# Kernel tuning notes

Measured on AMD Instinct MI355X. Metric: run time of the kernel, lower is better.

## Reference

```python
import jax, jax.numpy as jnp
import numpy as np
import math

B, S, D = 32, 512, 1024
H = 16
DH = D // H
L = 4
DFF = 2048
DMEM = 512
EPS = 1e-5


def _pos_encoding(seq_len, d_model):
    # sinusoidal PE, shape [seq_len, 1, d_model]
    position = jnp.arange(seq_len, dtype=jnp.float32)[:, None]
    div_term = jnp.exp(jnp.arange(0, d_model, 2, dtype=jnp.float32) * (-math.log(10000.0) / d_model))
    pe = jnp.zeros((seq_len, d_model), dtype=jnp.float32)
    pe = pe.at[:, 0::2].set(jnp.sin(position * div_term))
    pe = pe.at[:, 1::2].set(jnp.cos(position * div_term))
    return pe[:, None, :]


def _layer_norm(x, g, b):
    mu = jnp.mean(x, axis=-1, keepdims=True)
    var = jnp.mean(jnp.square(x - mu), axis=-1, keepdims=True)
    return (x - mu) * jax.lax.rsqrt(var + EPS) * g + b


def setup_inputs() -> dict:
    key = jax.random.key(0)
    ks = jax.random.split(key, 8)
    w = 0.02  # weight scale for stable deep stack
    return {
        "x": jax.random.normal(ks[0], (B, S, D), dtype=jnp.float32),
        "Wqkv": jax.random.normal(ks[1], (L, 3 * D, D), dtype=jnp.float32) * w,
        "bqkv": jnp.zeros((L, 3 * D), dtype=jnp.float32),
        "Wo": jax.random.normal(ks[2], (L, D, D), dtype=jnp.float32) * w,
        "bo": jnp.zeros((L, D), dtype=jnp.float32),
        "W1": jax.random.normal(ks[3], (L, DFF, D), dtype=jnp.float32) * w,
        "b1": jnp.zeros((L, DFF), dtype=jnp.float32),
        "W2": jax.random.normal(ks[4], (L, D, DFF), dtype=jnp.float32) * w,
        "b2": jnp.zeros((L, D), dtype=jnp.float32),
        "ln1_g": jnp.ones((L, D), dtype=jnp.float32),
        "ln1_b": jnp.zeros((L, D), dtype=jnp.float32),
        "ln2_g": jnp.ones((L, D), dtype=jnp.float32),
        "ln2_b": jnp.zeros((L, D), dtype=jnp.float32),
        "normf_g": jnp.ones((D,), dtype=jnp.float32),
        "normf_b": jnp.zeros((D,), dtype=jnp.float32),
        "Wout": jax.random.normal(ks[5], (DMEM, D), dtype=jnp.float32) * w,
        "bout": jnp.zeros((DMEM,), dtype=jnp.float32),
    }


def reference(x, Wqkv, bqkv, Wo, bo, W1, b1, W2, b2,
              ln1_g, ln1_b, ln2_g, ln2_b, normf_g, normf_b, Wout, bout):
    # x: [B, S, D] -> [S, B, D]
    h = jnp.transpose(x, (1, 0, 2))
    h = h + _pos_encoding(S, D)  # dropout p=0 in eval
    scale = 1.0 / math.sqrt(DH)
    for l in range(L):
        # --- self-attention block (post-norm) ---
        qkv = h @ Wqkv[l].T + bqkv[l]          # [S, B, 3D]
        q, k, v = jnp.split(qkv, 3, axis=-1)
        q = q.reshape(S, B, H, DH)
        k = k.reshape(S, B, H, DH)
        v = v.reshape(S, B, H, DH)
        scores = jnp.einsum('sbhd,tbhd->bhst', q, k) * scale  # [B, H, S, S]
        attn = jax.nn.softmax(scores, axis=-1)
        ctx = jnp.einsum('bhst,tbhd->sbhd', attn, v).reshape(S, B, D)
        sa = ctx @ Wo[l].T + bo[l]
        h = _layer_norm(h + sa, ln1_g[l], ln1_b[l])
        # --- feed-forward block (post-norm) ---
        ff = jax.nn.relu(h @ W1[l].T + b1[l]) @ W2[l].T + b2[l]
        h = _layer_norm(h + ff, ln2_g[l], ln2_b[l])
    h = _layer_norm(h, normf_g, normf_b)       # encoder final norm
    h = jnp.transpose(h, (1, 0, 2))            # [B, S, D]
    return h @ Wout.T + bout                   # [B, S, DMEM]
```

## Files before the change

kernel.cpp:

```cpp
#include <hip/hip_runtime.h>

#define BB    32
#define SS    512
#define DD    1024
#define HH_   16
#define DH    64
#define LL    4
#define DFF   2048
#define DMEM  512
#define NTOK  (BB * SS)
#define SPLD  74

typedef __attribute__((ext_vector_type(8))) short short8;
typedef __attribute__((ext_vector_type(4))) float f32x4;

__device__ __forceinline__ unsigned short f2bf(float x) {
    unsigned u = __float_as_uint(x);
    u = (u + 0x7FFFu + ((u >> 16) & 1u)) >> 16;
    return (unsigned short)u;
}
__device__ __forceinline__ float bf2f(unsigned short x) {
    return __uint_as_float(((unsigned)x) << 16);
}

__device__ __forceinline__ void async16(const unsigned short* g, unsigned short* l) {
    __builtin_amdgcn_global_load_lds(
        (__attribute__((address_space(1))) void*)g,
        (__attribute__((address_space(3))) void*)l,
        16, 0, 0);
}

__global__ void cvt_bf16(const float* __restrict__ in, unsigned short* __restrict__ out, int n) {
    int i4 = (blockIdx.x * 256 + threadIdx.x) * 4;
    if (i4 < n) {
        float4 v = *(const float4*)&in[i4];
        uint2 pk;
        pk.x = f2bf(v.x) | ((unsigned)f2bf(v.y) << 16);
        pk.y = f2bf(v.z) | ((unsigned)f2bf(v.w) << 16);
        *(uint2*)&out[i4] = pk;
    }
}

__global__ void add_pe_kernel(const float* __restrict__ x,
                              unsigned short* __restrict__ hb) {
    int i4 = (blockIdx.x * 256 + threadIdx.x) * 4;
    int d = i4 & (DD - 1);
    int t = i4 >> 10;
    int s = t & (SS - 1);
    const float c = -9.210340371976184f / (float)DD;
    float f0 = __expf((float)d * c);
    float f2 = __expf((float)(d + 2) * c);
    float a0 = (float)s * f0, a2 = (float)s * f2;
    float4 xv = *(const float4*)&x[i4];
    uint2 pk;
    pk.x = f2bf(xv.x + __sinf(a0)) | ((unsigned)f2bf(xv.y + __cosf(a0)) << 16);
    pk.y = f2bf(xv.z + __sinf(a2)) | ((unsigned)f2bf(xv.w + __cosf(a2)) << 16);
    *(uint2*)&hb[i4] = pk;
}

#define BAR   __builtin_amdgcn_s_barrier()
#define LGKM0 do { asm volatile("s_waitcnt lgkmcnt(0)" ::: "memory"); \
                   __builtin_amdgcn_sched_barrier(0); } while (0)
#define VMC8  asm volatile("s_waitcnt vmcnt(8)" ::: "memory")

#define STAGE(BUF, OP, HALFI, KS) do {                                          \
    const unsigned short* _g = (OP) ? Wb : A;                                   \
    const size_t _gr = ((OP) ? Brow0 : Arow0) + (HALFI) * 128 + wid * 16 + l8;  \
    unsigned short* _d = &lds[BUF][OP][(((HALFI) * 128 + wid * 16)) * 64];      \
    const int _ks = (KS);                                                       \
    async16(&_g[_gr * (size_t)K + _ks + cl8], _d);                              \
    async16(&_g[(_gr + 8) * (size_t)K + _ks + cl8], _d + 8 * 64);               \
} while (0)

#define HALF_ITER(CUR, KSR) {                                                   \
    short8 afr[4][2], b01[2][2], b23[2][2];                                     \
    _Pragma("unroll") for (int m = 0; m < 4; m++) {                             \
        afr[m][0] = *(const short8*)&lds[CUR][0][aro + m * 1024 + cb0];         \
        afr[m][1] = *(const short8*)&lds[CUR][0][aro + m * 1024 + cb1]; }       \
    _Pragma("unroll") for (int n = 0; n < 2; n++) {                             \
        b01[n][0] = *(const short8*)&lds[CUR][1][bro + n * 1024 + cb0];         \
        b01[n][1] = *(const short8*)&lds[CUR][1][bro + n * 1024 + cb1]; }       \
    BAR; LGKM0;                                                                 \
    __builtin_amdgcn_s_setprio(1);                                              \
    _Pragma("unroll") for (int m = 0; m < 4; m++)                               \
        _Pragma("unroll") for (int n = 0; n < 2; n++) {                         \
            acc[m][n] = __builtin_amdgcn_mfma_f32_16x16x32_bf16(b01[n][0], afr[m][0], acc[m][n], 0, 0, 0); \
            acc[m][n] = __builtin_amdgcn_mfma_f32_16x16x32_bf16(b01[n][1], afr[m][1], acc[m][n], 0, 0, 0); } \
    __builtin_amdgcn_s_setprio(0);                                              \
    BAR;                                                                        \
    _Pragma("unroll") for (int n = 0; n < 2; n++) {                             \
        b23[n][0] = *(const short8*)&lds[CUR][1][bro + (n + 2) * 1024 + cb0];   \
        b23[n][1] = *(const short8*)&lds[CUR][1][bro + (n + 2) * 1024 + cb1]; } \
    BAR; LGKM0;                                                                 \
    __builtin_amdgcn_s_setprio(1);                                              \
    _Pragma("unroll") for (int m = 0; m < 4; m++)                               \
        _Pragma("unroll") for (int n = 0; n < 2; n++) {                         \
            acc[m][n + 2] = __builtin_amdgcn_mfma_f32_16x16x32_bf16(b23[n][0], afr[m][0], acc[m][n + 2], 0, 0, 0); \
            acc[m][n + 2] = __builtin_amdgcn_mfma_f32_16x16x32_bf16(b23[n][1], afr[m][1], acc[m][n + 2], 0, 0, 0); } \
    __builtin_amdgcn_s_setprio(0);                                              \
    BAR;                                                                        \
    _Pragma("unroll") for (int m = 0; m < 4; m++) {                             \
        afr[m][0] = *(const short8*)&lds[CUR][0][aro + (m + 4) * 1024 + cb0];   \
        afr[m][1] = *(const short8*)&lds[CUR][0][aro + (m + 4) * 1024 + cb1]; } \
    STAGE(CUR, 1, 0, KSR);                                                      \
    STAGE(CUR, 1, 1, KSR);                                                      \
    BAR; LGKM0;                                                                 \
    __builtin_amdgcn_s_setprio(1);                                              \
    _Pragma("unroll") for (int m = 0; m < 4; m++)                               \
        _Pragma("unroll") for (int n = 0; n < 2; n++) {                         \
            acc[m + 4][n + 2] = __builtin_amdgcn_mfma_f32_16x16x32_bf16(b23[n][0], afr[m][0], acc[m + 4][n + 2], 0, 0, 0); \
            acc[m + 4][n + 2] = __builtin_amdgcn_mfma_f32_16x16x32_bf16(b23[n][1], afr[m][1], acc[m + 4][n + 2], 0, 0, 0); } \
    __builtin_amdgcn_s_setprio(0);                                              \
    BAR;                                                                        \
    STAGE(CUR, 0, 0, KSR);                                                      \
    STAGE(CUR, 0, 1, KSR);                                                      \
    VMC8;                                                                       \
    BAR;                                                                        \
    __builtin_amdgcn_s_setprio(1);                                              \
    _Pragma("unroll") for (int m = 0; m < 4; m++)                               \
        _Pragma("unroll") for (int n = 0; n < 2; n++) {                         \
            acc[m + 4][n] = __builtin_amdgcn_mfma_f32_16x16x32_bf16(b01[n][0], afr[m][0], acc[m + 4][n], 0, 0, 0); \
            acc[m + 4][n] = __builtin_amdgcn_mfma_f32_16x16x32_bf16(b01[n][1], afr[m][1], acc[m + 4][n], 0, 0, 0); } \
    __builtin_amdgcn_s_setprio(0);                                              \
    BAR;                                                                        \
}

template<bool RELU>
__global__ __launch_bounds__(512, 2) void gemm_bt8(
    const unsigned short* __restrict__ A,
    const unsigned short* __restrict__ Wb,
    const float* __restrict__ bias,
    float* __restrict__ Cf, unsigned short* __restrict__ Cb,
    int M, int N, int K)
{
    __shared__ __align__(16) unsigned short lds[2][2][256 * 64];
    const int tid  = threadIdx.x;
    const int wid  = tid >> 6, lane = tid & 63;
    const int wm   = wid >> 2, wn = wid & 3;
    const int quad = lane >> 4, l16 = lane & 15;
    const int l8   = lane >> 3;
    const int cl8  = (((lane & 7) ^ l8) & 7) * 8;

    const int nwgx = gridDim.x;
    const int nwg  = nwgx * (int)gridDim.y;
    int orig = blockIdx.y * nwgx + blockIdx.x;
    int swid = ((nwg & 7) == 0) ? ((orig & 7) * (nwg >> 3) + (orig >> 3)) : orig;
    const int bm = swid / nwgx, bn = swid % nwgx;
    const size_t Arow0 = (size_t)bm * 256, Brow0 = (size_t)bn * 256;

    const int swz = l16 & 7;
    const int cb0 = ((quad) ^ swz) * 8;
    const int cb1 = ((4 + quad) ^ swz) * 8;
    const int aro = (wm * 128 + l16) * 64;
    const int bro = (wn * 64 + l16) * 64;

    f32x4 acc[8][4];
    #pragma unroll
    for (int i = 0; i < 8; i++)
        #pragma unroll
        for (int j = 0; j < 4; j++) acc[i][j] = (f32x4){0.f, 0.f, 0.f, 0.f};

    STAGE(0, 1, 0, 0);  STAGE(0, 1, 1, 0);
    STAGE(0, 0, 0, 0);  STAGE(0, 0, 1, 0);
    STAGE(1, 1, 0, 64); STAGE(1, 1, 1, 64);
    STAGE(1, 0, 0, 64); STAGE(1, 0, 1, 64);
    VMC8;
    BAR;

    const int NT = K >> 6;
    for (int t = 0; t < NT; t += 2) {
        const int ks0 = ((t + 2 < NT) ? (t + 2) : (NT - 1)) * 64;
        const int ks1 = ((t + 3 < NT) ? (t + 3) : (NT - 1)) * 64;
        HALF_ITER(0, ks0)
        HALF_ITER(1, ks1)
    }

    #pragma unroll
    for (int i = 0; i < 8; i++) {
        const size_t mrow = (size_t)(bm * 256 + wm * 128 + i * 16 + l16) * N;
        #pragma unroll
        for (int j = 0; j < 4; j++) {
            int n0 = bn * 256 + wn * 64 + j * 16 + quad * 4;
            f32x4 av = acc[i][j];
            float v[4];
            if (bias) {
                float4 bv = *(const float4*)&bias[n0];
                v[0] = av[0] + bv.x; v[1] = av[1] + bv.y;
                v[2] = av[2] + bv.z; v[3] = av[3] + bv.w;
            } else {
                v[0] = av[0]; v[1] = av[1]; v[2] = av[2]; v[3] = av[3];
            }
            if (RELU) {
                #pragma unroll
                for (int r = 0; r < 4; r++) v[r] = fmaxf(v[r], 0.f);
            }
            if (Cf) {
                float4 o4; o4.x = v[0]; o4.y = v[1]; o4.z = v[2]; o4.w = v[3];
                *(float4*)&Cf[mrow + n0] = o4;
            }
            if (Cb) {
                uint2 pk;
                pk.x = f2bf(v[0]) | ((unsigned)f2bf(v[1]) << 16);
                pk.y = f2bf(v[2]) | ((unsigned)f2bf(v[3]) << 16);
                *(uint2*)&Cb[mrow + n0] = pk;
            }
        }
    }
}

template<bool RELU, bool WPRE>
__global__ __launch_bounds__(256) void gemm_bt(
    const unsigned short* __restrict__ A,
    const unsigned short* __restrict__ Wb,
    const float* __restrict__ Wf,
    const float* __restrict__ bias,
    float* __restrict__ Cf, unsigned short* __restrict__ Cb,
    int M, int N, int K)
{
    __shared__ __align__(16) unsigned short As[128 * 32];
    __shared__ __align__(16) unsigned short Bs[128 * 32];
    const int tid  = threadIdx.x;
    const int bm   = blockIdx.y, bn = blockIdx.x;
    const int w    = tid >> 6, lane = tid & 63;
    const int wm   = (w >> 1) * 64, wn = (w & 1) * 64;
    const int quad = lane >> 4, l16 = lane & 15;

    f32x4 acc[4][4];
    #pragma unroll
    for (int i = 0; i < 4; i++)
        #pragma unroll
        for (int j = 0; j < 4; j++) acc[i][j] = (f32x4){0.f, 0.f, 0.f, 0.f};

    const int rlane = lane >> 2, clane = (lane & 3) * 8;

    for (int k0 = 0; k0 < K; k0 += 32) {
        __syncthreads();
        if (WPRE) {
            #pragma unroll
            for (int i = 0; i < 2; i++) {
                int j = w * 2 + i;
                async16(&A [(size_t)(bm * 128 + j * 16 + rlane) * K + k0 + clane], &As[j * 512]);
                async16(&Wb[(size_t)(bn * 128 + j * 16 + rlane) * K + k0 + clane], &Bs[j * 512]);
            }
        } else {
            #pragma unroll
            for (int u = 0; u < 2; u++) {
                int c = tid * 2 + u;
                int row = c >> 2, cc = (c & 3) * 8;
                *(uint4*)&As[row * 32 + cc] =
                    *(const uint4*)&A[(size_t)(bm * 128 + row) * K + k0 + cc];
                const float* wp = &Wf[(size_t)(bn * 128 + row) * K + k0 + cc];
                float4 w0 = *(const float4*)wp;
                float4 w1 = *(const float4*)(wp + 4);
                uint4 pk;
                pk.x = ((unsigned)f2bf(w0.y) << 16) | f2bf(w0.x);
                pk.y = ((unsigned)f2bf(w0.w) << 16) | f2bf(w0.z);
                pk.z = ((unsigned)f2bf(w1.y) << 16) | f2bf(w1.x);
                pk.w = ((unsigned)f2bf(w1.w) << 16) | f2bf(w1.z);
                *(uint4*)&Bs[row * 32 + cc] = pk;
            }
        }
        __syncthreads();
        short8 af[4], bfr[4];
        #pragma unroll
        for (int i = 0; i < 4; i++)
            af[i] = *(const short8*)&As[(wm + i * 16 + l16) * 32 + quad * 8];
        #pragma unroll
        for (int j = 0; j < 4; j++)
            bfr[j] = *(const short8*)&Bs[(wn + j * 16 + l16) * 32 + quad * 8];
        #pragma unroll
        for (int i = 0; i < 4; i++)
            #pragma unroll
            for (int j = 0; j < 4; j++)
                acc[i][j] = __builtin_amdgcn_mfma_f32_16x16x32_bf16(bfr[j], af[i], acc[i][j], 0, 0, 0);
    }

    #pragma unroll
    for (int i = 0; i < 4; i++) {
        const size_t mrow = (size_t)(bm * 128 + wm + i * 16 + l16) * N;
        #pragma unroll
        for (int j = 0; j < 4; j++) {
            int n0 = bn * 128 + wn + j * 16 + quad * 4;
            f32x4 av = acc[i][j];
            float v[4];
            if (bias) {
                float4 bv = *(const float4*)&bias[n0];
                v[0] = av[0] + bv.x; v[1] = av[1] + bv.y;
                v[2] = av[2] + bv.z; v[3] = av[3] + bv.w;
            } else {
                v[0] = av[0]; v[1] = av[1]; v[2] = av[2]; v[3] = av[3];
            }
            if (RELU) {
                #pragma unroll
                for (int r = 0; r < 4; r++) v[r] = fmaxf(v[r], 0.f);
            }
            if (Cf) {
                float4 o4; o4.x = v[0]; o4.y = v[1]; o4.z = v[2]; o4.w = v[3];
                *(float4*)&Cf[mrow + n0] = o4;
            }
            if (Cb) {
                uint2 pk;
                pk.x = f2bf(v[0]) | ((unsigned)f2bf(v[1]) << 16);
                pk.y = f2bf(v[2]) | ((unsigned)f2bf(v[3]) << 16);
                *(uint2*)&Cb[mrow + n0] = pk;
            }
        }
    }
}

__global__ __launch_bounds__(256) void attn_kernel(const unsigned short* __restrict__ qkv,
                                                   unsigned short* __restrict__ ctx)
{
    __shared__ __align__(16) unsigned short sK [64 * SPLD];
    __shared__ __align__(16) unsigned short sVt[64 * SPLD];
    __shared__ __align__(16) unsigned short sP [128 * SPLD];

    const int tid  = threadIdx.x;
    const int blk  = blockIdx.x;
    const int qt   = blk & 3;
    const int hh   = (blk >> 2) & 15;
    const int b    = blk >> 6;
    const int w    = tid >> 6, lane = tid & 63;
    const int quad = lane >> 4, l16 = lane & 15;
    const size_t rowbase = (size_t)b * SS;
    const int LDQ = 3 * DD;

    short8 qf[2][2];
    #pragma unroll
    for (int m = 0; m < 2; m++) {
        const unsigned short* qrow =
            qkv + (rowbase + qt * 128 + w * 32 + m * 16 + l16) * (size_t)LDQ + hh * 64;
        #pragma unroll
        for (int kk = 0; kk < 2; kk++) {
            uint4 q4 = *(const uint4*)&qrow[kk * 32 + quad * 8];
            unsigned short* qs = (unsigned short*)&q4;
            short8 f;
            short* fp = (short*)&f;
            #pragma unroll
            for (int e = 0; e < 8; e++) fp[e] = (short)f2bf(bf2f(qs[e]) * 0.125f);
            qf[m][kk] = f;
        }
    }

    float l_part[2] = {0.f, 0.f};
    f32x4 o[2][4];
    #pragma unroll
    for (int m = 0; m < 2; m++)
        #pragma unroll
        for (int nt = 0; nt < 4; nt++) o[m][nt] = (f32x4){0.f, 0.f, 0.f, 0.f};

    for (int kt = 0; kt < 8; kt++) {
        __syncthreads();
        #pragma unroll
        for (int u = 0; u < 2; u++) {
            int c = tid * 2 + u;
            int r = c >> 3, cc = (c & 7) * 8;
            const size_t src = (rowbase + kt * 64 + r) * (size_t)LDQ + hh * 64 + cc;
            *(uint4*)&sK[r * SPLD + cc] = *(const uint4*)&qkv[src + DD];
            uint4 v4 = *(const uint4*)&qkv[src + 2 * DD];
            unsigned short* vs = (unsigned short*)&v4;
            #pragma unroll
            for (int e = 0; e < 8; e++) sVt[(cc + e) * SPLD + r] = vs[e];
        }
        __syncthreads();

        #pragma unroll
        for (int m = 0; m < 2; m++) {
            f32x4 s[4];
            #pragma unroll
            for (int ct = 0; ct < 4; ct++) s[ct] = (f32x4){0.f, 0.f, 0.f, 0.f};
            #pragma unroll
            for (int kk = 0; kk < 2; kk++)
                #pragma unroll
                for (int ct = 0; ct < 4; ct++) {
                    short8 kb = *(const short8*)&sK[(ct * 16 + l16) * SPLD + kk * 32 + quad * 8];
                    s[ct] = __builtin_amdgcn_mfma_f32_16x16x32_bf16(kb, qf[m][kk], s[ct], 0, 0, 0);
                }
            const int prow = (w * 32 + m * 16 + l16) * SPLD;
            float lp = 0.f;
            #pragma unroll
            for (int ct = 0; ct < 4; ct++) {
                float p0 = __expf(fminf(s[ct][0], 30.f));
                float p1 = __expf(fminf(s[ct][1], 30.f));
                float p2 = __expf(fminf(s[ct][2], 30.f));
                float p3 = __expf(fminf(s[ct][3], 30.f));
                lp += (p0 + p1) + (p2 + p3);
                uint2 pk;
                pk.x = f2bf(p0) | ((unsigned)f2bf(p1) << 16);
                pk.y = f2bf(p2) | ((unsigned)f2bf(p3) << 16);
                *(uint2*)&sP[prow + ct * 16 + quad * 4] = pk;
            }
            l_part[m] += lp;
        }

        #pragma unroll
        for (int m = 0; m < 2; m++)
            #pragma unroll
            for (int kk = 0; kk < 2; kk++) {
                short8 pa = *(const short8*)&sP[(w * 32 + m * 16 + l16) * SPLD + kk * 32 + quad * 8];
                #pragma unroll
                for (int nt = 0; nt < 4; nt++) {
                    short8 vb = *(const short8*)&sVt[(nt * 16 + l16) * SPLD + kk * 32 + quad * 8];
                    o[m][nt] = __builtin_amdgcn_mfma_f32_16x16x32_bf16(vb, pa, o[m][nt], 0, 0, 0);
                }
            }
    }

    #pragma unroll
    for (int m = 0; m < 2; m++) {
        float lt = l_part[m];
        lt += __shfl_xor(lt, 16);
        lt += __shfl_xor(lt, 32);
        float inv = 1.f / lt;
        const size_t crow = (rowbase + qt * 128 + w * 32 + m * 16 + l16) * DD + hh * 64;
        #pragma unroll
        for (int nt = 0; nt < 4; nt++) {
            uint2 pk;
            pk.x = f2bf(o[m][nt][0] * inv) | ((unsigned)f2bf(o[m][nt][1] * inv) << 16);
            pk.y = f2bf(o[m][nt][2] * inv) | ((unsigned)f2bf(o[m][nt][3] * inv) << 16);
            *(uint2*)&ctx[crow + nt * 16 + quad * 4] = pk;
        }
    }
}

__global__ __launch_bounds__(256) void ln_kernel(
    unsigned short* __restrict__ hb, const unsigned short* __restrict__ add,
    const float* __restrict__ g, const float* __restrict__ beta)
{
    __shared__ float sred[4];
    const int t = blockIdx.x, tid = threadIdx.x;
    const int d0 = tid * 4;
    const size_t base = (size_t)t * DD + d0;
    float x[4];
    {
        uint2 hv = *(const uint2*)&hb[base];
        x[0] = bf2f(hv.x & 0xFFFF); x[1] = bf2f(hv.x >> 16);
        x[2] = bf2f(hv.y & 0xFFFF); x[3] = bf2f(hv.y >> 16);
    }
    if (add) {
        uint2 av = *(const uint2*)&add[base];
        x[0] += bf2f(av.x & 0xFFFF); x[1] += bf2f(av.x >> 16);
        x[2] += bf2f(av.y & 0xFFFF); x[3] += bf2f(av.y >> 16);
    }
    float s = (x[0] + x[1]) + (x[2] + x[3]);
    #pragma unroll
    for (int off = 32; off > 0; off >>= 1) s += __shfl_down(s, off);
    if ((tid & 63) == 0) sred[tid >> 6] = s;
    __syncthreads();
    float mu = (sred[0] + sred[1] + sred[2] + sred[3]) * (1.f / DD);
    __syncthreads();
    float vs = 0.f;
    #pragma unroll
    for (int i = 0; i < 4; i++) { float dx = x[i] - mu; vs += dx * dx; }
    #pragma unroll
    for (int off = 32; off > 0; off >>= 1) vs += __shfl_down(vs, off);
    if ((tid & 63) == 0) sred[tid >> 6] = vs;
    __syncthreads();
    float var = (sred[0] + sred[1] + sred[2] + sred[3]) * (1.f / DD);
    float inv = rsqrtf(var + 1e-5f);
    float4 gv = *(const float4*)&g[d0];
    float4 bv = *(const float4*)&beta[d0];
    float y0 = (x[0] - mu) * inv * gv.x + bv.x;
    float y1 = (x[1] - mu) * inv * gv.y + bv.y;
    float y2 = (x[2] - mu) * inv * gv.z + bv.z;
    float y3 = (x[3] - mu) * inv * gv.w + bv.w;
    uint2 pk;
    pk.x = f2bf(y0) | ((unsigned)f2bf(y1) << 16);
    pk.y = f2bf(y2) | ((unsigned)f2bf(y3) << 16);
    *(uint2*)&hb[base] = pk;
}

static void launch_gemm(bool relu, bool pre, const unsigned short* A,
                        const unsigned short* Wb, const float* Wf, const float* bias,
                        float* Cf, unsigned short* Cb, int M, int N, int K, hipStream_t s)
{
    if (pre && (M % 256 == 0) && (N % 256 == 0) && (K % 128 == 0) && N >= 1024) {
        dim3 g8(N / 256, M / 256);
        if (relu) gemm_bt8<true ><<<g8, 512, 0, s>>>(A, Wb, bias, Cf, Cb, M, N, K);
        else      gemm_bt8<false><<<g8, 512, 0, s>>>(A, Wb, bias, Cf, Cb, M, N, K);
        return;
    }
    dim3 g(N / 128, M / 128);
    if (pre) {
        if (relu) gemm_bt<true,  true ><<<g, 256, 0, s>>>(A, Wb, nullptr, bias, Cf, Cb, M, N, K);
        else      gemm_bt<false, true ><<<g, 256, 0, s>>>(A, Wb, nullptr, bias, Cf, Cb, M, N, K);
    } else {
        if (relu) gemm_bt<true,  false><<<g, 256, 0, s>>>(A, nullptr, Wf, bias, Cf, Cb, M, N, K);
        else      gemm_bt<false, false><<<g, 256, 0, s>>>(A, nullptr, Wf, bias, Cf, Cb, M, N, K);
    }
}

extern "C" void kernel_launch(void* const* d_in, const int* in_sizes, int n_in,
                              void* d_out, int out_size, void* d_ws, size_t ws_size,
                              hipStream_t stream)
{
    const float* x    = (const float*)d_in[0];
    const float* Wqkv = (const float*)d_in[1];
    const float* bqkv = (const float*)d_in[2];
    const float* Wo   = (const float*)d_in[3];
    const float* bo   = (const float*)d_in[4];
    const float* W1   = (const float*)d_in[5];
    const float* b1   = (const float*)d_in[6];
    const float* W2   = (const float*)d_in[7];
    const float* b2   = (const float*)d_in[8];
    const float* ln1g = (const float*)d_in[9];
    const float* ln1b = (const float*)d_in[10];
    const float* ln2g = (const float*)d_in[11];
    const float* ln2b = (const float*)d_in[12];
    const float* nfg  = (const float*)d_in[13];
    const float* nfb  = (const float*)d_in[14];
    const float* Wout = (const float*)d_in[15];
    const float* bout = (const float*)d_in[16];
    float* out = (float*)d_out;

    char* ws = (char*)d_ws;
    const size_t MB = 1024 * 1024;
    unsigned short* hb    = (unsigned short*)(ws + 0 * MB);
    unsigned short* qkvb  = (unsigned short*)(ws + 32 * MB);
    unsigned short* tmpb  = (unsigned short*)(ws + 96 * MB);
    unsigned short* ctxb  = (unsigned short*)(ws + 128 * MB);
    unsigned short* WqkvB = (unsigned short*)(ws + 160 * MB);
    unsigned short* W1B   = (unsigned short*)(ws + 184 * MB);
    unsigned short* W2B   = (unsigned short*)(ws + 200 * MB);
    unsigned short* WoB   = (unsigned short*)(ws + 216 * MB);
    unsigned short* WoutB = (unsigned short*)(ws + 224 * MB);

    const bool pre = ws_size >= 225 * MB;
    if (pre) {
        cvt_bf16<<<(LL * 3 * DD * DD / 4 + 255) / 256, 256, 0, stream>>>(Wqkv, WqkvB, LL * 3 * DD * DD);
        cvt_bf16<<<(LL * DFF * DD / 4 + 255) / 256, 256, 0, stream>>>(W1, W1B, LL * DFF * DD);
        cvt_bf16<<<(LL * DD * DFF / 4 + 255) / 256, 256, 0, stream>>>(W2, W2B, LL * DD * DFF);
        cvt_bf16<<<(LL * DD * DD / 4 + 255) / 256, 256, 0, stream>>>(Wo, WoB, LL * DD * DD);
        cvt_bf16<<<(DMEM * DD / 4 + 255) / 256, 256, 0, stream>>>(Wout, WoutB, DMEM * DD);
    }

    add_pe_kernel<<<NTOK * DD / 1024, 256, 0, stream>>>(x, hb);

    for (int l = 0; l < LL; l++) {
        launch_gemm(false, pre, hb, WqkvB + (size_t)l * 3 * DD * DD,
                    Wqkv + (size_t)l * 3 * DD * DD, bqkv + l * 3 * DD,
                    nullptr, qkvb, NTOK, 3 * DD, DD, stream);
        attn_kernel<<<BB * HH_ * 4, 256, 0, stream>>>(qkvb, ctxb);
        launch_gemm(false, pre, ctxb, WoB + (size_t)l * DD * DD,
                    Wo + (size_t)l * DD * DD, bo + l * DD,
                    nullptr, tmpb, NTOK, DD, DD, stream);
        ln_kernel<<<NTOK, 256, 0, stream>>>(hb, tmpb, ln1g + l * DD, ln1b + l * DD);
        launch_gemm(true, pre, hb, W1B + (size_t)l * DFF * DD,
                    W1 + (size_t)l * DFF * DD, b1 + l * DFF,
                    nullptr, qkvb, NTOK, DFF, DD, stream);
        launch_gemm(false, pre, qkvb, W2B + (size_t)l * DD * DFF,
                    W2 + (size_t)l * DD * DFF, b2 + l * DD,
                    nullptr, tmpb, NTOK, DD, DFF, stream);
        ln_kernel<<<NTOK, 256, 0, stream>>>(hb, tmpb, ln2g + l * DD, ln2b + l * DD);
    }
    ln_kernel<<<NTOK, 256, 0, stream>>>(hb, nullptr, nfg, nfb);
    launch_gemm(false, pre, hb, WoutB, Wout, bout, out, nullptr, NTOK, DMEM, DD, stream);
}
```

Before: 2.025 ms.

## Add finer-grained prefetch GEMM variant for wide-N projections without block swizzle

After: 2.064 ms, median of 2. Within noise of the previous version (+1.9%).

```diff
diff --git a/kernel.cpp b/kernel.cpp
--- a/kernel.cpp
+++ b/kernel.cpp
@@ -61,6 +61,7 @@
 #define BAR   __builtin_amdgcn_s_barrier()
 #define LGKM0 do { asm volatile("s_waitcnt lgkmcnt(0)" ::: "memory"); \
                    __builtin_amdgcn_sched_barrier(0); } while (0)
+#define VMC4  asm volatile("s_waitcnt vmcnt(4)" ::: "memory")
 #define VMC8  asm volatile("s_waitcnt vmcnt(8)" ::: "memory")
 
 #define STAGE(BUF, OP, HALFI, KS) do {                                          \
@@ -72,7 +73,60 @@
     async16(&_g[(_gr + 8) * (size_t)K + _ks + cl8], _d + 8 * 64);               \
 } while (0)
 
-#define HALF_ITER(CUR, KSR) {                                                   \
+#define HALF_ITER_A(CUR, OTH, KS1, KS2) {                                       \
+    short8 afr[4][2], b01[2][2], b23[2][2];                                     \
+    _Pragma("unroll") for (int m = 0; m < 4; m++) {                             \
+        afr[m][0] = *(const short8*)&lds[CUR][0][aro + m * 1024 + cb0];         \
+        afr[m][1] = *(const short8*)&lds[CUR][0][aro + m * 1024 + cb1]; }       \
+    _Pragma("unroll") for (int n = 0; n < 2; n++) {                             \
+        b01[n][0] = *(const short8*)&lds[CUR][1][bro + n * 1024 + cb0];         \
+        b01[n][1] = *(const short8*)&lds[CUR][1][bro + n * 1024 + cb1]; }       \
+    STAGE(OTH, 0, 0, KS1);                                                      \
+    BAR; LGKM0;                                                                 \
+    __builtin_amdgcn_s_setprio(1);                                              \
+    _Pragma("unroll") for (int m = 0; m < 4; m++)                               \
+        _Pragma("unroll") for (int n = 0; n < 2; n++) {                         \
+            acc[m][n] = __builtin_amdgcn_mfma_f32_16x16x32_bf16(b01[n][0], afr[m][0], acc[m][n], 0, 0, 0); \
+            acc[m][n] = __builtin_amdgcn_mfma_f32_16x16x32_bf16(b01[n][1], afr[m][1], acc[m][n], 0, 0, 0); } \
+    __builtin_amdgcn_s_setprio(0);                                              \
+    BAR;                                                                        \
+    _Pragma("unroll") for (int n = 0; n < 2; n++) {                             \
+        b23[n][0] = *(const short8*)&lds[CUR][1][bro + (n + 2) * 1024 + cb0];   \
+        b23[n][1] = *(const short8*)&lds[CUR][1][bro + (n + 2) * 1024 + cb1]; } \
+    STAGE(OTH, 0, 1, KS1);                                                      \
+    BAR; LGKM0;                                                                 \
+    __builtin_amdgcn_s_setprio(1);                                              \
+    _Pragma("unroll") for (int m = 0; m < 4; m++)                               \
+        _Pragma("unroll") for (int n = 0; n < 2; n++) {                         \
+            acc[m][n + 2] = __builtin_amdgcn_mfma_f32_16x16x32_bf16(b23[n][0], afr[m][0], acc[m][n + 2], 0, 0, 0); \
+            acc[m][n + 2] = __builtin_amdgcn_mfma_f32_16x16x32_bf16(b23[n][1], afr[m][1], acc[m][n + 2], 0, 0, 0); } \
+    __builtin_amdgcn_s_setprio(0);                                              \
+    BAR;                                                                        \
+    _Pragma("unroll") for (int m = 0; m < 4; m++) {                             \
+        afr[m][0] = *(const short8*)&lds[CUR][0][aro + (m + 4) * 1024 + cb0];   \
+        afr[m][1] = *(const short8*)&lds[CUR][0][aro + (m + 4) * 1024 + cb1]; } \
+    STAGE(CUR, 1, 0, KS2);                                                      \
+    BAR; LGKM0;                                                                 \
+    __builtin_amdgcn_s_setprio(1);                                              \
+    _Pragma("unroll") for (int m = 0; m < 4; m++)                               \
+        _Pragma("unroll") for (int n = 0; n < 2; n++) {                         \
+            acc[m + 4][n + 2] = __builtin_amdgcn_mfma_f32_16x16x32_bf16(b23[n][0], afr[m][0], acc[m + 4][n + 2], 0, 0, 0); \
+            acc[m + 4][n + 2] = __builtin_amdgcn_mfma_f32_16x16x32_bf16(b23[n][1], afr[m][1], acc[m + 4][n + 2], 0, 0, 0); } \
+    __builtin_amdgcn_s_setprio(0);                                              \
+    BAR;                                                                        \
+    STAGE(CUR, 1, 1, KS2);                                                      \
+    VMC4;                                                                       \
+    BAR;                                                                        \
+    __builtin_amdgcn_s_setprio(1);                                              \
+    _Pragma("unroll") for (int m = 0; m < 4; m++)                               \
+        _Pragma("unroll") for (int n = 0; n < 2; n++) {                         \
+            acc[m + 4][n] = __builtin_amdgcn_mfma_f32_16x16x32_bf16(b01[n][0], afr[m][0], acc[m + 4][n], 0, 0, 0); \
+            acc[m + 4][n] = __builtin_amdgcn_mfma_f32_16x16x32_bf16(b01[n][1], afr[m][1], acc[m + 4][n], 0, 0, 0); } \
+    __builtin_amdgcn_s_setprio(0);                                              \
+    BAR;                                                                        \
+}
+
+#define HALF_ITER_B(CUR, KSR) {                                                 \
     short8 afr[4][2], b01[2][2], b23[2][2];                                     \
     _Pragma("unroll") for (int m = 0; m < 4; m++) {                             \
         afr[m][0] = *(const short8*)&lds[CUR][0][aro + m * 1024 + cb0];         \
@@ -125,8 +179,41 @@
     BAR;                                                                        \
 }
 
+#define GEMM_EPILOGUE                                                           \
+    _Pragma("unroll")                                                           \
+    for (int i = 0; i < 8; i++) {                                               \
+        const size_t mrow = (size_t)(bm * 256 + wm * 128 + i * 16 + l16) * N;   \
+        _Pragma("unroll")                                                       \
+        for (int j = 0; j < 4; j++) {                                           \
+            int n0 = bn * 256 + wn * 64 + j * 16 + quad * 4;                    \
+            f32x4 av = acc[i][j];                                               \
+            float v[4];                                                         \
+            if (bias) {                                                         \
+                float4 bv = *(const float4*)&bias[n0];                          \
+                v[0] = av[0] + bv.x; v[1] = av[1] + bv.y;                       \
+                v[2] = av[2] + bv.z; v[3] = av[3] + bv.w;                       \
+            } else {                                                            \
+                v[0] = av[0]; v[1] = av[1]; v[2] = av[2]; v[3] = av[3];         \
+            }                                                                   \
+            if (RELU) {                                                         \
+                _Pragma("unroll")                                               \
+                for (int r = 0; r < 4; r++) v[r] = fmaxf(v[r], 0.f);            \
+            }                                                                   \
+            if (Cf) {                                                           \
+                float4 o4; o4.x = v[0]; o4.y = v[1]; o4.z = v[2]; o4.w = v[3];  \
+                *(float4*)&Cf[mrow + n0] = o4;                                  \
+            }                                                                   \
+            if (Cb) {                                                           \
+                uint2 pk;                                                       \
+                pk.x = f2bf(v[0]) | ((unsigned)f2bf(v[1]) << 16);               \
+                pk.y = f2bf(v[2]) | ((unsigned)f2bf(v[3]) << 16);               \
+                *(uint2*)&Cb[mrow + n0] = pk;                                   \
+            }                                                                   \
+        }                                                                       \
+    }
+
 template<bool RELU>
-__global__ __launch_bounds__(512, 2) void gemm_bt8(
+__global__ __launch_bounds__(512, 2) void gemm_bt8a(
     const unsigned short* __restrict__ A,
     const unsigned short* __restrict__ Wb,
     const float* __restrict__ bias,
@@ -140,6 +227,52 @@
     const int quad = lane >> 4, l16 = lane & 15;
     const int l8   = lane >> 3;
     const int cl8  = (((lane & 7) ^ l8) & 7) * 8;
+    const int bm   = blockIdx.y, bn = blockIdx.x;
+    const size_t Arow0 = (size_t)bm * 256, Brow0 = (size_t)bn * 256;
+
+    const int swz = l16 & 7;
+    const int cb0 = ((quad) ^ swz) * 8;
+    const int cb1 = ((4 + quad) ^ swz) * 8;
+    const int aro = (wm * 128 + l16) * 64;
+    const int bro = (wn * 64 + l16) * 64;
+
+    f32x4 acc[8][4];
+    #pragma unroll
+    for (int i = 0; i < 8; i++)
+        #pragma unroll
+        for (int j = 0; j < 4; j++) acc[i][j] = (f32x4){0.f, 0.f, 0.f, 0.f};
+
+    STAGE(0, 1, 0, 0);  STAGE(0, 1, 1, 0);
+    STAGE(0, 0, 0, 0);  STAGE(0, 0, 1, 0);
+    STAGE(1, 1, 0, 64); STAGE(1, 1, 1, 64);
+    VMC4;
+    BAR;
+
+    for (int k0 = 0; k0 < K; k0 += 128) {
+        const int ksb = (k0 + 128 < K) ? (k0 + 128) : (K - 64);
+        const int ksc = (k0 + 192 < K) ? (k0 + 192) : (K - 64);
+        HALF_ITER_A(0, 1, k0 + 64, ksb)
+        HALF_ITER_A(1, 0, ksb, ksc)
+    }
+
+    GEMM_EPILOGUE
+}
+
+template<bool RELU>
+__global__ __launch_bounds__(512, 2) void gemm_bt8b(
+    const unsigned short* __restrict__ A,
+    const unsigned short* __restrict__ Wb,
+    const float* __restrict__ bias,
+    float* __restrict__ Cf, unsigned short* __restrict__ Cb,
+    int M, int N, int K)
+{
+    __shared__ __align__(16) unsigned short lds[2][2][256 * 64];
+    const int tid  = threadIdx.x;
+    const int wid  = tid >> 6, lane = tid & 63;
+    const int wm   = wid >> 2, wn = wid & 3;
+    const int quad = lane >> 4, l16 = lane & 15;
+    const int l8   = lane >> 3;
+    const int cl8  = (((lane & 7) ^ l8) & 7) * 8;
 
     const int nwgx = gridDim.x;
     const int nwg  = nwgx * (int)gridDim.y;
@@ -171,41 +304,11 @@
     for (int t = 0; t < NT; t += 2) {
         const int ks0 = ((t + 2 < NT) ? (t + 2) : (NT - 1)) * 64;
         const int ks1 = ((t + 3 < NT) ? (t + 3) : (NT - 1)) * 64;
-        HALF_ITER(0, ks0)
-        HALF_ITER(1, ks1)
-    }
-
-    #pragma unroll
-    for (int i = 0; i < 8; i++) {
-        const size_t mrow = (size_t)(bm * 256 + wm * 128 + i * 16 + l16) * N;
-        #pragma unroll
-        for (int j = 0; j < 4; j++) {
-            int n0 = bn * 256 + wn * 64 + j * 16 + quad * 4;
-            f32x4 av = acc[i][j];
-            float v[4];
-            if (bias) {
-                float4 bv = *(const float4*)&bias[n0];
-                v[0] = av[0] + bv.x; v[1] = av[1] + bv.y;
-                v[2] = av[2] + bv.z; v[3] = av[3] + bv.w;
-            } else {
-                v[0] = av[0]; v[1] = av[1]; v[2] = av[2]; v[3] = av[3];
-            }
-            if (RELU) {
-                #pragma unroll
-                for (int r = 0; r < 4; r++) v[r] = fmaxf(v[r], 0.f);
-            }
-            if (Cf) {
-                float4 o4; o4.x = v[0]; o4.y = v[1]; o4.z = v[2]; o4.w = v[3];
-                *(float4*)&Cf[mrow + n0] = o4;
-            }
-            if (Cb) {
-                uint2 pk;
-                pk.x = f2bf(v[0]) | ((unsigned)f2bf(v[1]) << 16);
-                pk.y = f2bf(v[2]) | ((unsigned)f2bf(v[3]) << 16);
-                *(uint2*)&Cb[mrow + n0] = pk;
-            }
-        }
-    }
+        HALF_ITER_B(0, ks0)
+        HALF_ITER_B(1, ks1)
+    }
+
+    GEMM_EPILOGUE
 }
 
 template<bool RELU, bool WPRE>
@@ -476,8 +579,13 @@
 {
     if (pre && (M % 256 == 0) && (N % 256 == 0) && (K % 128 == 0) && N >= 1024) {
         dim3 g8(N / 256, M / 256);
-        if (relu) gemm_bt8<true ><<<g8, 512, 0, s>>>(A, Wb, bias, Cf, Cb, M, N, K);
-        else      gemm_bt8<false><<<g8, 512, 0, s>>>(A, Wb, bias, Cf, Cb, M, N, K);
+        if (N >= 3072) {
+            if (relu) gemm_bt8a<true ><<<g8, 512, 0, s>>>(A, Wb, bias, Cf, Cb, M, N, K);
+            else      gemm_bt8a<false><<<g8, 512, 0, s>>>(A, Wb, bias, Cf, Cb, M, N, K);
+        } else {
+            if (relu) gemm_bt8b<true ><<<g8, 512, 0, s>>>(A, Wb, bias, Cf, Cb, M, N, K);
+            else      gemm_bt8b<false><<<g8, 512, 0, s>>>(A, Wb, bias, Cf, Cb, M, N, K);
+        }
         return;
     }
     dim3 g(N / 128, M / 128);
```
